# Performance work log

Measured on AMD Instinct MI355X. Metric: run time of the kernel, lower is better.

The kernel has to match this reference:

```python
import jax, jax.numpy as jnp
import numpy as np

HEADS = 4
DIM_HEAD = 32
SCALE = 10.0
EPS = 1e-12  # F.normalize eps


def setup_inputs() -> dict:
    key = jax.random.key(0)
    k0, k1, k2 = jax.random.split(key, 3)
    b, c, h, w = 4, 256, 64, 64
    hidden = HEADS * DIM_HEAD  # 128
    x = jax.random.normal(k0, (b, c, h, w), dtype=jnp.float32)
    # 1x1 convs == per-pixel linear layers; store as [out_ch, in_ch]
    w_qkv = jax.random.normal(k1, (3 * hidden, c), dtype=jnp.float32) * (1.0 / np.sqrt(c))
    w_out = jax.random.normal(k2, (c, hidden), dtype=jnp.float32) * (1.0 / np.sqrt(hidden))
    b_out = jnp.zeros((c,), dtype=jnp.float32)
    return {"x": x, "w_qkv": w_qkv, "w_out": w_out, "b_out": b_out}


def _l2norm(t):
    # normalize along the per-head feature dim d (axis=2 of [b,h,d,n])
    n = jnp.sqrt(jnp.sum(t * t, axis=2, keepdims=True))
    return t / jnp.maximum(n, EPS)


def reference(x, w_qkv, w_out, b_out):
    b, c, h, w = x.shape
    n = h * w
    # to_qkv 1x1 conv (no bias)
    qkv = jnp.einsum('oc,bchw->bohw', w_qkv, x)          # [b, 3*hidden, h, w]
    qkv = qkv.reshape(b, 3, HEADS, DIM_HEAD, n)          # chunk dim=1 then split heads
    q, k, v = qkv[:, 0], qkv[:, 1], qkv[:, 2]            # each [b, heads, d, n]
    q = _l2norm(q)
    k = _l2norm(k)
    sim = jnp.einsum('bhdi,bhdj->bhij', q, k) * SCALE    # [b, heads, n, n]
    attn = jax.nn.softmax(sim, axis=-1)
    out = jnp.einsum('bhij,bhdj->bhid', attn, v)         # [b, heads, n, d]
    # 'b h (x y) d -> b (h d) x y'
    out = out.transpose(0, 1, 3, 2).reshape(b, HEADS * DIM_HEAD, h, w)
    # to_out 1x1 conv with bias
    return jnp.einsum('oc,bchw->bohw', w_out, out) + b_out[None, :, None, None]
```

## Files before the change

### kernel.cpp

```cpp
#include <hip/hip_runtime.h>
#include <math.h>

#define BB 4
#define CC 256
#define NHEAD 4
#define DH 32
#define NN 4096
#define HID 128

typedef _Float16 f16;
typedef _Float16 f16x8 __attribute__((ext_vector_type(8)));
typedef _Float16 f16x4 __attribute__((ext_vector_type(4)));
typedef float f32x4 __attribute__((ext_vector_type(4)));
typedef unsigned int u32x4 __attribute__((ext_vector_type(4)));

#define QPRESCALE 14.42695041f
#define NSHIFT 14.42695041f

#if __has_builtin(__builtin_amdgcn_exp2f)
#define EXP2F(x) __builtin_amdgcn_exp2f(x)
#else
#define EXP2F(x) __expf((x)*0.6931471805599453f)
#endif

__device__ __forceinline__ f16x8 cvt8(const float* p) {
    float4 a = *(const float4*)p;
    float4 b = *(const float4*)(p + 4);
    f16x8 r;
    r[0] = (f16)a.x; r[1] = (f16)a.y; r[2] = (f16)a.z; r[3] = (f16)a.w;
    r[4] = (f16)b.x; r[5] = (f16)b.y; r[6] = (f16)b.z; r[7] = (f16)b.w;
    return r;
}

#define XROW 40

__global__ __launch_bounds__(256) void qkv_mega(const float* __restrict__ x,
                                                const float* __restrict__ wq,
                                                f16* __restrict__ qh,
                                                f16* __restrict__ kh,
                                                f16* __restrict__ vh) {
    __shared__ __align__(16) f16 xl[32 * XROW];
    int t = threadIdx.x;
    int wave = t >> 6, lane = t & 63;
    int quad = lane >> 4, col = lane & 15;
    int b = blockIdx.z;
    int i0 = blockIdx.x * 32;
    int o0w = wave * 96;

    int sc = t >> 3;
    int iseg = t & 7;
    const float* xb = x + (size_t)b * CC * NN + i0 + iseg * 4;

    f32x4 c[6][2];
#pragma unroll
    for (int mt = 0; mt < 6; mt++)
#pragma unroll
        for (int nt = 0; nt < 2; nt++) c[mt][nt] = f32x4{0.f, 0.f, 0.f, 0.f};

#pragma unroll
    for (int k0 = 0; k0 < CC; k0 += 32) {
        float4 xv = *(const float4*)(xb + (size_t)(k0 + sc) * NN);
        __syncthreads();
        xl[(iseg * 4 + 0) * XROW + sc] = (f16)xv.x;
        xl[(iseg * 4 + 1) * XROW + sc] = (f16)xv.y;
        xl[(iseg * 4 + 2) * XROW + sc] = (f16)xv.z;
        xl[(iseg * 4 + 3) * XROW + sc] = (f16)xv.w;
        __syncthreads();
        f16x8 bf0 = *(const f16x8*)(xl + (size_t)col * XROW + quad * 8);
        f16x8 bf1 = *(const f16x8*)(xl + (size_t)(16 + col) * XROW + quad * 8);
#pragma unroll
        for (int mt = 0; mt < 6; mt++) {
            f16x8 a = cvt8(wq + (size_t)(o0w + mt * 16 + col) * CC + k0 + quad * 8);
            c[mt][0] = __builtin_amdgcn_mfma_f32_16x16x32_f16(a, bf0, c[mt][0], 0, 0, 0);
            c[mt][1] = __builtin_amdgcn_mfma_f32_16x16x32_f16(a, bf1, c[mt][1], 0, 0, 0);
        }
    }

#pragma unroll
    for (int hh = 0; hh < 3; hh++) {
        int oh = o0w + hh * 32;
        if (oh < 256) {
            int isQ = (oh < 128);
            f16* dst = isQ ? qh : kh;
            int h = (isQ ? oh : (oh - 128)) >> 5;
            float pre = isQ ? QPRESCALE : 1.0f;
#pragma unroll
            for (int nt = 0; nt < 2; nt++) {
                float ss = 0.f;
#pragma unroll
                for (int m2 = 0; m2 < 2; m2++)
#pragma unroll
                    for (int r = 0; r < 4; r++) {
                        float v = c[hh * 2 + m2][nt][r];
                        ss = fmaf(v, v, ss);
                    }
                ss += __shfl_xor(ss, 16);
                ss += __shfl_xor(ss, 32);
                float inv = pre / fmaxf(sqrtf(ss), 1e-12f);
                size_t row = ((size_t)(b * 4 + h) * NN + i0 + nt * 16 + col) * 32;
#pragma unroll
                for (int m2 = 0; m2 < 2; m2++) {
                    f16x4 st;
#pragma unroll
                    for (int r = 0; r < 4; r++) st[r] = (f16)(c[hh * 2 + m2][nt][r] * inv);
                    *(f16x4*)(dst + row + m2 * 16 + quad * 4) = st;
                }
            }
        } else {
            int h = (oh - 256) >> 5;
#pragma unroll
            for (int nt = 0; nt < 2; nt++) {
                int i = i0 + nt * 16 + col;
#pragma unroll
                for (int m2 = 0; m2 < 2; m2++)
#pragma unroll
                    for (int r = 0; r < 4; r++)
                        vh[((size_t)(b * 4 + h) * 32 + m2 * 16 + quad * 4 + r) * NN + i] =
                            (f16)c[hh * 2 + m2][nt][r];
            }
        }
    }
}

#define KROW 40
#define VROW 72

__device__ __forceinline__ f16x8 expblk2(f32x4 sa, f32x4 sb) {
    u32x4 w;
    w[0] = __builtin_bit_cast(unsigned int,
            __builtin_amdgcn_cvt_pkrtz(EXP2F(sa[0]), EXP2F(sa[1])));
    w[1] = __builtin_bit_cast(unsigned int,
            __builtin_amdgcn_cvt_pkrtz(EXP2F(sa[2]), EXP2F(sa[3])));
    w[2] = __builtin_bit_cast(unsigned int,
            __builtin_amdgcn_cvt_pkrtz(EXP2F(sb[0]), EXP2F(sb[1])));
    w[3] = __builtin_bit_cast(unsigned int,
            __builtin_amdgcn_cvt_pkrtz(EXP2F(sb[2]), EXP2F(sb[3])));
    return __builtin_bit_cast(f16x8, w);
}

__device__ __forceinline__ void compute_g(const f16* kl, const f16* vl, int jb,
                                          int col, int quad, const f16x8 (&qB)[4],
                                          f32x4 (&o)[4][2], f32x4 (&lf)[4]) {
    f16x8 kA = *(const f16x8*)(kl + (jb + col) * KROW + quad * 8);
    f16x8 kB = *(const f16x8*)(kl + (jb + 16 + col) * KROW + quad * 8);
    f16x8 v0 = *(const f16x8*)(vl + col * VROW + jb + quad * 8);
    f16x8 v1 = *(const f16x8*)(vl + (16 + col) * VROW + jb + quad * 8);
    const f32x4 zs = {-NSHIFT, -NSHIFT, -NSHIFT, -NSHIFT};
    f16 one = (f16)1.0f;
    f16x8 ones = {one, one, one, one, one, one, one, one};
#pragma unroll
    for (int f = 0; f < 4; f++) {
        f32x4 sa = __builtin_amdgcn_mfma_f32_16x16x32_f16(kA, qB[f], zs, 0, 0, 0);
        f32x4 sb = __builtin_amdgcn_mfma_f32_16x16x32_f16(kB, qB[f], zs, 0, 0, 0);
        f16x8 p = expblk2(sa, sb);
        o[f][0] = __builtin_amdgcn_mfma_f32_16x16x32_f16(p, v0, o[f][0], 0, 0, 0);
        o[f][1] = __builtin_amdgcn_mfma_f32_16x16x32_f16(p, v1, o[f][1], 0, 0, 0);
        lf[f]   = __builtin_amdgcn_mfma_f32_16x16x32_f16(p, ones, lf[f], 0, 0, 0);
    }
}

template <int SPLIT>
__global__ __launch_bounds__(256, 4) void attn_mfma(const f16* __restrict__ qh,
                                                    const f16* __restrict__ kh,
                                                    const f16* __restrict__ vh,
                                                    float* __restrict__ op,
                                                    float* __restrict__ lp,
                                                    f16* __restrict__ att16) {
    __shared__ __align__(16) f16 klds[2][64 * KROW];
    __shared__ __align__(16) f16 vlds[2][32 * VROW];
    int t = threadIdx.x;
    int wave = t >> 6, lane = t & 63;
    int quad = lane >> 4, col = lane & 15;

    int bid = blockIdx.x;
    int xcd = bid & 7;
    int slot = bid >> 3;
    int bh = xcd * 2 + slot / (16 * SPLIT);
    int rem = slot % (16 * SPLIT);
    int s = rem >> 4;
    int i0 = (rem & 15) * 256;
    int iw = i0 + wave * 64;

    const int NT = 64 / SPLIT;
    int kbase = s * (NN / SPLIT);

    const f16* qb = qh + (size_t)bh * NN * 32;
    const f16* kb = kh + (size_t)bh * NN * 32 + (size_t)kbase * 32;
    const f16* vb = vh + (size_t)bh * 32 * NN + kbase;

    f16x8 qB[4];
#pragma unroll
    for (int f = 0; f < 4; f++)
        qB[f] = *(const f16x8*)(qb + (size_t)(iw + f * 16 + col) * 32 + quad * 8);

    f32x4 o[4][2], lf[4];
#pragma unroll
    for (int f = 0; f < 4; f++) {
        o[f][0] = f32x4{0.f, 0.f, 0.f, 0.f};
        o[f][1] = f32x4{0.f, 0.f, 0.f, 0.f};
        lf[f]   = f32x4{0.f, 0.f, 0.f, 0.f};
    }

    int ktr = t >> 2, kts = t & 3;
    int ksrc = (ktr & 32) | ((ktr & 12) << 1) | ((ktr & 16) >> 2) | (ktr & 3);
    int vtr = t >> 3, vts = t & 7;

    f16x8 kr, vr;
    kr = *(const f16x8*)(kb + (size_t)(0 + ksrc) * 32 + kts * 8);
    vr = *(const f16x8*)(vb + (size_t)vtr * NN + 0 + vts * 8);
    *(f16x8*)(&klds[0][0] + ktr * KROW + kts * 8) = kr;
    *(f16x8*)(&vlds[0][0] + vtr * VROW + vts * 8) = vr;
    __syncthreads();
    kr = *(const f16x8*)(kb + (size_t)(64 + ksrc) * 32 + kts * 8);
    vr = *(const f16x8*)(vb + (size_t)vtr * NN + 64 + vts * 8);

    for (int tile = 0; tile < NT - 2; tile++) {
        int buf = tile & 1;
        const f16* kl = &klds[buf][0];
        const f16* vl = &vlds[buf][0];
        compute_g(kl, vl, 0, col, quad, qB, o, lf);
        compute_g(kl, vl, 32, col, quad, qB, o, lf);
        *(f16x8*)(&klds[buf ^ 1][0] + ktr * KROW + kts * 8) = kr;
        *(f16x8*)(&vlds[buf ^ 1][0] + vtr * VROW + vts * 8) = vr;
        __syncthreads();
        int j0 = (tile + 2) * 64;
        kr = *(const f16x8*)(kb + (size_t)(j0 + ksrc) * 32 + kts * 8);
        vr = *(const f16x8*)(vb + (size_t)vtr * NN + j0 + vts * 8);
    }
    {
        compute_g(&klds[0][0], &vlds[0][0], 0, col, quad, qB, o, lf);
        compute_g(&klds[0][0], &vlds[0][0], 32, col, quad, qB, o, lf);
        *(f16x8*)(&klds[1][0] + ktr * KROW + kts * 8) = kr;
        *(f16x8*)(&vlds[1][0] + vtr * VROW + vts * 8) = vr;
        __syncthreads();
    }
    {
        compute_g(&klds[1][0], &vlds[1][0], 0, col, quad, qB, o, lf);
        compute_g(&klds[1][0], &vlds[1][0], 32, col, quad, qB, o, lf);
    }

    if constexpr (SPLIT == 1) {
        int b = bh >> 2, h = bh & 3;
        f16* ab = att16 + (size_t)b * NN * HID + h * 32;
#pragma unroll
        for (int f = 0; f < 4; f++)
#pragma unroll
            for (int r = 0; r < 4; r++) {
                float inv = __builtin_amdgcn_rcpf(lf[f][r]);
                size_t row = (size_t)(iw + f * 16 + quad * 4 + r) * HID;
                ab[row + col]      = (f16)(o[f][0][r] * inv);
                ab[row + 16 + col] = (f16)(o[f][1][r] * inv);
            }
    } else {
        float* ob = op + (size_t)(s * 16 + bh) * NN * 32;
#pragma unroll
        for (int f = 0; f < 4; f++)
#pragma unroll
            for (int r = 0; r < 4; r++) {
                size_t rr = (size_t)(iw + f * 16 + quad * 4 + r) * 32;
                ob[rr + col]      = o[f][0][r];
                ob[rr + 16 + col] = o[f][1][r];
            }
        if (col == 0) {
            float* lb = lp + (size_t)(s * 16 + bh) * NN;
#pragma unroll
            for (int f = 0; f < 4; f++)
#pragma unroll
                for (int r = 0; r < 4; r++)
                    lb[iw + f * 16 + quad * 4 + r] = lf[f][r];
        }
    }
}

__global__ __launch_bounds__(256) void attn_combine(const float* __restrict__ op,
                                                    const float* __restrict__ lp,
                                                    f16* __restrict__ att16,
                                                    int nsplit) {
    int gid = blockIdx.x * 256 + threadIdx.x;
    int rowid = gid >> 3;
    int seg = gid & 7;
    int bh = rowid >> 12;
    int q = rowid & 4095;

    float l = 0.f;
    f32x4 acc = {0.f, 0.f, 0.f, 0.f};
    for (int s = 0; s < nsplit; s++) {
        l += lp[(size_t)(s * 16 + bh) * NN + q];
        f32x4 a = *(const f32x4*)(op + ((size_t)(s * 16 + bh) * NN + q) * 32 + seg * 4);
        acc += a;
    }
    float inv = __builtin_amdgcn_rcpf(l);
    int b = bh >> 2, h = bh & 3;
    f16x4 st;
    st[0] = (f16)(acc[0] * inv);
    st[1] = (f16)(acc[1] * inv);
    st[2] = (f16)(acc[2] * inv);
    st[3] = (f16)(acc[3] * inv);
    *(f16x4*)(att16 + ((size_t)b * NN + q) * HID + h * 32 + seg * 4) = st;
}

__global__ __launch_bounds__(256) void out_mfma(const f16* __restrict__ att16,
                                                const float* __restrict__ wo,
                                                const float* __restrict__ bo,
                                                float* __restrict__ out) {
    int wave = threadIdx.x >> 6, lane = threadIdx.x & 63;
    int quad = lane >> 4, col = lane & 15;
    int b = blockIdx.z;
    int i0 = (blockIdx.x * 4 + wave) * 32;
    int o0 = blockIdx.y * 64;
    const f16* ab = att16 + (size_t)b * NN * HID;

    const f32x4 z = {0.f, 0.f, 0.f, 0.f};
    f32x4 c[2][4];
#pragma unroll
    for (int it = 0; it < 2; it++)
#pragma unroll
        for (int ot = 0; ot < 4; ot++) c[it][ot] = z;

#pragma unroll
    for (int k0 = 0; k0 < HID; k0 += 32) {
        f16x8 a0 = *(const f16x8*)(ab + (size_t)(i0 + col) * HID + k0 + quad * 8);
        f16x8 a1 = *(const f16x8*)(ab + (size_t)(i0 + 16 + col) * HID + k0 + quad * 8);
#pragma unroll
        for (int ot = 0; ot < 4; ot++) {
            f16x8 bf = cvt8(wo + (size_t)(o0 + ot * 16 + col) * HID + k0 + quad * 8);
            c[0][ot] = __builtin_amdgcn_mfma_f32_16x16x32_f16(a0, bf, c[0][ot], 0, 0, 0);
            c[1][ot] = __builtin_amdgcn_mfma_f32_16x16x32_f16(a1, bf, c[1][ot], 0, 0, 0);
        }
    }

#pragma unroll
    for (int it = 0; it < 2; it++)
#pragma unroll
        for (int ot = 0; ot < 4; ot++) {
            int o = o0 + ot * 16 + col;
            float bias = bo[o];
            int i = i0 + it * 16 + quad * 4;
            float4 st = {c[it][ot][0] + bias, c[it][ot][1] + bias,
                         c[it][ot][2] + bias, c[it][ot][3] + bias};
            *(float4*)(out + ((size_t)b * CC + o) * NN + i) = st;
        }
}

extern "C" void kernel_launch(void* const* d_in, const int* in_sizes, int n_in,
                              void* d_out, int out_size, void* d_ws, size_t ws_size,
                              hipStream_t stream) {
    const float* x     = (const float*)d_in[0];
    const float* w_qkv = (const float*)d_in[1];
    const float* w_out = (const float*)d_in[2];
    const float* b_out = (const float*)d_in[3];
    float* out = (float*)d_out;

    char* ws = (char*)d_ws;
    f16* qh    = (f16*)(ws);
    f16* kh    = (f16*)(ws + (4u << 20));
    f16* vh    = (f16*)(ws + (8u << 20));
    f16* att16 = (f16*)(ws + (12u << 20));

    qkv_mega<<<dim3(NN / 32, 1, BB), 256, 0, stream>>>(x, w_qkv, qh, kh, vh);

    if (ws_size >= (50ull << 20)) {
        float* op = (float*)(ws + (16ull << 20));
        float* lp = (float*)(ws + (48ull << 20));
        attn_mfma<4><<<dim3(1024), 256, 0, stream>>>(qh, kh, vh, op, lp, att16);
        attn_combine<<<dim3(2048), 256, 0, stream>>>(op, lp, att16, 4);
    } else if (ws_size >= (33ull << 20)) {
        float* op = (float*)(ws + (16ull << 20));
        float* lp = (float*)(ws + (32ull << 20));
        attn_mfma<2><<<dim3(512), 256, 0, stream>>>(qh, kh, vh, op, lp, att16);
        attn_combine<<<dim3(2048), 256, 0, stream>>>(op, lp, att16, 2);
    } else {
        attn_mfma<1><<<dim3(256), 256, 0, stream>>>(qh, kh, vh, nullptr, nullptr, att16);
    }

    out_mfma<<<dim3(NN / 128, CC / 64, BB), 256, 0, stream>>>(att16, w_out, b_out, out);
}
```

Measured before the change: 153.5 us.

## Split QKV projection across output-channel blocks and stage output weights in LDS

After: 151.2 us. About the same (-1.5%).

```diff
diff --git a/kernel.cpp b/kernel.cpp
--- a/kernel.cpp
+++ b/kernel.cpp
@@ -34,26 +34,26 @@
 
 #define XROW 40
 
-__global__ __launch_bounds__(256) void qkv_mega(const float* __restrict__ x,
-                                                const float* __restrict__ wq,
-                                                f16* __restrict__ qh,
-                                                f16* __restrict__ kh,
-                                                f16* __restrict__ vh) {
+__global__ __launch_bounds__(256, 4) void qkv_mega(const float* __restrict__ x,
+                                                   const float* __restrict__ wq,
+                                                   f16* __restrict__ qh,
+                                                   f16* __restrict__ kh,
+                                                   f16* __restrict__ vh) {
     __shared__ __align__(16) f16 xl[32 * XROW];
     int t = threadIdx.x;
     int wave = t >> 6, lane = t & 63;
     int quad = lane >> 4, col = lane & 15;
     int b = blockIdx.z;
     int i0 = blockIdx.x * 32;
-    int o0w = wave * 96;
+    int o0w = blockIdx.y * 128 + wave * 32;
 
     int sc = t >> 3;
     int iseg = t & 7;
     const float* xb = x + (size_t)b * CC * NN + i0 + iseg * 4;
 
-    f32x4 c[6][2];
-#pragma unroll
-    for (int mt = 0; mt < 6; mt++)
+    f32x4 c[2][2];
+#pragma unroll
+    for (int mt = 0; mt < 2; mt++)
 #pragma unroll
         for (int nt = 0; nt < 2; nt++) c[mt][nt] = f32x4{0.f, 0.f, 0.f, 0.f};
 
@@ -69,55 +69,51 @@
         f16x8 bf0 = *(const f16x8*)(xl + (size_t)col * XROW + quad * 8);
         f16x8 bf1 = *(const f16x8*)(xl + (size_t)(16 + col) * XROW + quad * 8);
 #pragma unroll
-        for (int mt = 0; mt < 6; mt++) {
+        for (int mt = 0; mt < 2; mt++) {
             f16x8 a = cvt8(wq + (size_t)(o0w + mt * 16 + col) * CC + k0 + quad * 8);
             c[mt][0] = __builtin_amdgcn_mfma_f32_16x16x32_f16(a, bf0, c[mt][0], 0, 0, 0);
             c[mt][1] = __builtin_amdgcn_mfma_f32_16x16x32_f16(a, bf1, c[mt][1], 0, 0, 0);
         }
     }
 
-#pragma unroll
-    for (int hh = 0; hh < 3; hh++) {
-        int oh = o0w + hh * 32;
-        if (oh < 256) {
-            int isQ = (oh < 128);
-            f16* dst = isQ ? qh : kh;
-            int h = (isQ ? oh : (oh - 128)) >> 5;
-            float pre = isQ ? QPRESCALE : 1.0f;
-#pragma unroll
-            for (int nt = 0; nt < 2; nt++) {
-                float ss = 0.f;
-#pragma unroll
-                for (int m2 = 0; m2 < 2; m2++)
-#pragma unroll
-                    for (int r = 0; r < 4; r++) {
-                        float v = c[hh * 2 + m2][nt][r];
-                        ss = fmaf(v, v, ss);
-                    }
-                ss += __shfl_xor(ss, 16);
-                ss += __shfl_xor(ss, 32);
-                float inv = pre / fmaxf(sqrtf(ss), 1e-12f);
-                size_t row = ((size_t)(b * 4 + h) * NN + i0 + nt * 16 + col) * 32;
-#pragma unroll
-                for (int m2 = 0; m2 < 2; m2++) {
-                    f16x4 st;
-#pragma unroll
-                    for (int r = 0; r < 4; r++) st[r] = (f16)(c[hh * 2 + m2][nt][r] * inv);
-                    *(f16x4*)(dst + row + m2 * 16 + quad * 4) = st;
+    if (blockIdx.y < 2) {
+        int isQ = (blockIdx.y == 0);
+        f16* dst = isQ ? qh : kh;
+        int h = wave;
+        float pre = isQ ? QPRESCALE : 1.0f;
+#pragma unroll
+        for (int nt = 0; nt < 2; nt++) {
+            float ss = 0.f;
+#pragma unroll
+            for (int m2 = 0; m2 < 2; m2++)
+#pragma unroll
+                for (int r = 0; r < 4; r++) {
+                    float v = c[m2][nt][r];
+                    ss = fmaf(v, v, ss);
                 }
+            ss += __shfl_xor(ss, 16);
+            ss += __shfl_xor(ss, 32);
+            float inv = pre / fmaxf(sqrtf(ss), 1e-12f);
+            size_t row = ((size_t)(b * 4 + h) * NN + i0 + nt * 16 + col) * 32;
+#pragma unroll
+            for (int m2 = 0; m2 < 2; m2++) {
+                f16x4 st;
+#pragma unroll
+                for (int r = 0; r < 4; r++) st[r] = (f16)(c[m2][nt][r] * inv);
+                *(f16x4*)(dst + row + m2 * 16 + quad * 4) = st;
             }
-        } else {
-            int h = (oh - 256) >> 5;
-#pragma unroll
-            for (int nt = 0; nt < 2; nt++) {
-                int i = i0 + nt * 16 + col;
-#pragma unroll
-                for (int m2 = 0; m2 < 2; m2++)
-#pragma unroll
-                    for (int r = 0; r < 4; r++)
-                        vh[((size_t)(b * 4 + h) * 32 + m2 * 16 + quad * 4 + r) * NN + i] =
-                            (f16)c[hh * 2 + m2][nt][r];
-            }
+        }
+    } else {
+        int h = wave;
+#pragma unroll
+        for (int nt = 0; nt < 2; nt++) {
+            int i = i0 + nt * 16 + col;
+#pragma unroll
+            for (int m2 = 0; m2 < 2; m2++)
+#pragma unroll
+                for (int r = 0; r < 4; r++)
+                    vh[((size_t)(b * 4 + h) * 32 + m2 * 16 + quad * 4 + r) * NN + i] =
+                        (f16)c[m2][nt][r];
         }
     }
 }
@@ -299,47 +295,62 @@
     *(f16x4*)(att16 + ((size_t)b * NN + q) * HID + h * 32 + seg * 4) = st;
 }
 
-__global__ __launch_bounds__(256) void out_mfma(const f16* __restrict__ att16,
-                                                const float* __restrict__ wo,
-                                                const float* __restrict__ bo,
-                                                float* __restrict__ out) {
-    int wave = threadIdx.x >> 6, lane = threadIdx.x & 63;
+#define WROW 136
+
+__global__ __launch_bounds__(256, 4) void out_mfma(const f16* __restrict__ att16,
+                                                   const float* __restrict__ wo,
+                                                   const float* __restrict__ bo,
+                                                   float* __restrict__ out) {
+    __shared__ __align__(16) f16 wol[64 * WROW];
+    int t = threadIdx.x;
+    int wave = t >> 6, lane = t & 63;
     int quad = lane >> 4, col = lane & 15;
     int b = blockIdx.z;
-    int i0 = (blockIdx.x * 4 + wave) * 32;
+    int i0w = blockIdx.x * 64 + wave * 16;
     int o0 = blockIdx.y * 64;
     const f16* ab = att16 + (size_t)b * NN * HID;
 
+    {
+        int row = t >> 2;
+        int kq = (t & 3) * 32;
+        const float* src = wo + (size_t)(o0 + row) * HID + kq;
+        f16* d = wol + row * WROW + kq;
+#pragma unroll
+        for (int j = 0; j < 4; j++) {
+            float4 a = *(const float4*)(src + j * 8);
+            float4 bq = *(const float4*)(src + j * 8 + 4);
+            f16x8 s;
+            s[0] = (f16)a.x; s[1] = (f16)a.y; s[2] = (f16)a.z; s[3] = (f16)a.w;
+            s[4] = (f16)bq.x; s[5] = (f16)bq.y; s[6] = (f16)bq.z; s[7] = (f16)bq.w;
+            *(f16x8*)(d + j * 8) = s;
+        }
+    }
+    __syncthreads();
+
     const f32x4 z = {0.f, 0.f, 0.f, 0.f};
-    f32x4 c[2][4];
-#pragma unroll
-    for (int it = 0; it < 2; it++)
-#pragma unroll
-        for (int ot = 0; ot < 4; ot++) c[it][ot] = z;
+    f32x4 c[4];
+#pragma unroll
+    for (int ot = 0; ot < 4; ot++) c[ot] = z;
 
 #pragma unroll
     for (int k0 = 0; k0 < HID; k0 += 32) {
-        f16x8 a0 = *(const f16x8*)(ab + (size_t)(i0 + col) * HID + k0 + quad * 8);
-        f16x8 a1 = *(const f16x8*)(ab + (size_t)(i0 + 16 + col) * HID + k0 + quad * 8);
+        f16x8 a0 = *(const f16x8*)(ab + (size_t)(i0w + col) * HID + k0 + quad * 8);
 #pragma unroll
         for (int ot = 0; ot < 4; ot++) {
-            f16x8 bf = cvt8(wo + (size_t)(o0 + ot * 16 + col) * HID + k0 + quad * 8);
-            c[0][ot] = __builtin_amdgcn_mfma_f32_16x16x32_f16(a0, bf, c[0][ot], 0, 0, 0);
-            c[1][ot] = __builtin_amdgcn_mfma_f32_16x16x32_f16(a1, bf, c[1][ot], 0, 0, 0);
-        }
-    }
-
-#pragma unroll
-    for (int it = 0; it < 2; it++)
-#pragma unroll
-        for (int ot = 0; ot < 4; ot++) {
-            int o = o0 + ot * 16 + col;
-            float bias = bo[o];
-            int i = i0 + it * 16 + quad * 4;
-            float4 st = {c[it][ot][0] + bias, c[it][ot][1] + bias,
-                         c[it][ot][2] + bias, c[it][ot][3] + bias};
-            *(float4*)(out + ((size_t)b * CC + o) * NN + i) = st;
-        }
+            f16x8 bf = *(const f16x8*)(wol + (size_t)(ot * 16 + col) * WROW + k0 + quad * 8);
+            c[ot] = __builtin_amdgcn_mfma_f32_16x16x32_f16(a0, bf, c[ot], 0, 0, 0);
+        }
+    }
+
+#pragma unroll
+    for (int ot = 0; ot < 4; ot++) {
+        int o = o0 + ot * 16 + col;
+        float bias = bo[o];
+        int i = i0w + quad * 4;
+        float4 st = {c[ot][0] + bias, c[ot][1] + bias,
+                     c[ot][2] + bias, c[ot][3] + bias};
+        *(float4*)(out + ((size_t)b * CC + o) * NN + i) = st;
+    }
 }
 
 extern "C" void kernel_launch(void* const* d_in, const int* in_sizes, int n_in,
@@ -357,7 +368,7 @@
     f16* vh    = (f16*)(ws + (8u << 20));
     f16* att16 = (f16*)(ws + (12u << 20));
 
-    qkv_mega<<<dim3(NN / 32, 1, BB), 256, 0, stream>>>(x, w_qkv, qh, kh, vh);
+    qkv_mega<<<dim3(NN / 32, 3, BB), 256, 0, stream>>>(x, w_qkv, qh, kh, vh);
 
     if (ws_size >= (50ull << 20)) {
         float* op = (float*)(ws + (16ull << 20));
@@ -373,5 +384,5 @@
         attn_mfma<1><<<dim3(256), 256, 0, stream>>>(qh, kh, vh, nullptr, nullptr, att16);
     }
 
-    out_mfma<<<dim3(NN / 128, CC / 64, BB), 256, 0, stream>>>(att16, w_out, b_out, out);
-}
+    out_mfma<<<dim3(NN / 64, CC / 64, BB), 256, 0, stream>>>(att16, w_out, b_out, out);
+}
```
